# Kernel optimization log

Measured on AMD Instinct MI355X. Metric: run time of the kernel, lower is better.

## Reference

```python
import jax, jax.numpy as jnp
import numpy as np

BLOCK_SIZE = 32
BITS = 4
Q_MAX = 2 ** (BITS - 1) - 1  # 7


def setup_inputs() -> dict:
    key = jax.random.key(0)
    k1, k2, k3, k4 = jax.random.split(key, 4)
    B, S, D_in, D_out = 4, 2048, 4096, 4096
    x = jax.random.normal(k1, (B, S, D_in), dtype=jnp.float32)
    # 4-bit symmetric quantized values in [-8, 7], stored as int32
    weight_q = jax.random.randint(k2, (D_out, D_in), -(2 ** (BITS - 1)), 2 ** (BITS - 1), dtype=jnp.int32)
    # per-block positive scales (abs-max of each block in the original)
    block_scales = jax.random.uniform(k3, (D_out, D_in // BLOCK_SIZE), dtype=jnp.float32, minval=0.01, maxval=1.0)
    bias = jax.random.normal(k4, (D_out,), dtype=jnp.float32) * 0.01
    return {"x": x, "weight_q": weight_q, "block_scales": block_scales, "bias": bias}


def _dequantize(weight_q, block_scales):
    out_f, in_f = weight_q.shape
    n_blocks = in_f // BLOCK_SIZE
    q = weight_q.reshape(out_f, n_blocks, BLOCK_SIZE).astype(jnp.float32)
    w = q / Q_MAX * block_scales[:, :, None]
    return w.reshape(out_f, in_f)


def reference(x, weight_q, block_scales, bias):
    # block dequantize: w = q / q_max * scale, then y = x @ w.T + b
    w = _dequantize(weight_q, block_scales)  # [out, in] fp32
    return jnp.einsum('bsi,oi->bso', x, w) + bias
```

## Files before the change

kernel.cpp:

```cpp
#include <hip/hip_runtime.h>
#include <stdint.h>

#define M_DIM 8192
#define N_DIM 4096
#define K_DIM 4096
#define NBLK  (K_DIM / 32)

typedef __attribute__((ext_vector_type(4)))  float          f32x4;
typedef __attribute__((ext_vector_type(16))) float          f32x16;
typedef __attribute__((ext_vector_type(8)))  short          bf16x8;
typedef __attribute__((ext_vector_type(4)))  int            i32x4;
typedef __attribute__((ext_vector_type(8)))  unsigned short u16x8;
typedef __attribute__((address_space(3)))    unsigned short lds_us;

__device__ __forceinline__ unsigned short f2bf(float f) {
  unsigned u = __builtin_bit_cast(unsigned, f);
  u += 0x7fffu + ((u >> 16) & 1u);
  return (unsigned short)(u >> 16);
}

__device__ __forceinline__ void stage16(const unsigned short* g, lds_us* l) {
  __builtin_amdgcn_global_load_lds(
      (const __attribute__((address_space(1))) void*)g,
      (__attribute__((address_space(3))) void*)l, 16, 0, 0);
}

template <int OFF>
__device__ __forceinline__ bf16x8 dsr(lds_us* addr) {
  bf16x8 d;
  asm volatile("ds_read_b128 %0, %1 offset:%2" : "=v"(d) : "v"(addr), "n"(OFF));
  return d;
}


__global__ void MXFP4_dequant_kernel(const int* __restrict__ wq,
                                     const float* __restrict__ scales,
                                     unsigned short* __restrict__ wb) {
  size_t t = (size_t)blockIdx.x * 256 + threadIdx.x;
  int l  = (int)(t & 63);
  int r  = l & 31, cq = l >> 5;
  int sub = (int)(t >> 6) & 15;
  int mb = sub >> 2, ks = sub & 3;
  int H = (int)(t >> 10) & 31;
  int g = (int)(t >> 15);
  size_t row = (size_t)H * 128 + mb * 32 + r;
  size_t k   = (size_t)g * 64 + ks * 16 + cq * 8;
  float s = scales[row * NBLK + (k >> 5)] * (1.0f / 7.0f);
  const int* src = wq + row * K_DIM + k;
  i32x4 q0 = *(const i32x4*)src;
  i32x4 q1 = *(const i32x4*)(src + 4);
  u16x8 out;
#pragma unroll
  for (int j = 0; j < 4; ++j) out[j]     = f2bf((float)q0[j] * s);
#pragma unroll
  for (int j = 0; j < 4; ++j) out[4 + j] = f2bf((float)q1[j] * s);
  *(u16x8*)(wb + t * 8) = out;
}

__global__ void MXFP4_cvt_kernel(const float* __restrict__ x,
                                 unsigned short* __restrict__ xb) {
  size_t t = (size_t)blockIdx.x * 256 + threadIdx.x;
  int l  = (int)(t & 63);
  int r  = l & 31, cq = l >> 5;
  int sub = (int)(t >> 6) & 15;
  int mb = sub >> 2, ks = sub & 3;
  int H = (int)(t >> 10) & 63;
  int g = (int)(t >> 16);
  size_t row = (size_t)H * 128 + mb * 32 + r;
  size_t k   = (size_t)g * 64 + ks * 16 + cq * 8;
  const float* src = x + row * K_DIM + k;
  f32x4 v0 = *(const f32x4*)src;
  f32x4 v1 = *(const f32x4*)(src + 4);
  u16x8 out;
#pragma unroll
  for (int j = 0; j < 4; ++j) out[j]     = f2bf(v0[j]);
#pragma unroll
  for (int j = 0; j < 4; ++j) out[4 + j] = f2bf(v1[j]);
  *(u16x8*)(xb + t * 8) = out;
}


#define BAR() __builtin_amdgcn_s_barrier()
#define WAIT_LGKM(N_) do { asm volatile("s_waitcnt lgkmcnt(%0)" :: "n"(N_) : "memory"); \
                           __builtin_amdgcn_sched_barrier(0); } while (0)

#define ST_A(t_, h_, BUFA_, valid_) do { \
  if (valid_) { \
    const unsigned short* s_ = Abase + ((size_t)(t_) * 64 + (h_)) * 8192 + tid8; \
    lds_us* d_ = lp + (BUFA_) * 16384 + (h_) * 8192 + tid8; \
    stage16(s_, d_); stage16(s_ + 4096, d_ + 4096); \
  } else { stage16(Abase + tid8, lp + 65536); \
           stage16(Abase + tid8 + 4096, lp + 65536 + 512); } \
} while (0)

#define ST_B(t_, h_, BUFB_, valid_) do { \
  if (valid_) { \
    const unsigned short* s_ = Bbase + ((size_t)(t_) * 32 + (h_)) * 8192 + tid8; \
    lds_us* d_ = lp + 32768 + (BUFB_) * 16384 + (h_) * 8192 + tid8; \
    stage16(s_, d_); stage16(s_ + 4096, d_ + 4096); \
  } else { stage16(Bbase + tid8, lp + 65536); \
           stage16(Bbase + tid8 + 4096, lp + 65536 + 512); } \
} while (0)

#define MF(MB_, NB_, AF_, BF_) do { \
  _Pragma("unroll") \
  for (int ks_ = 0; ks_ < 4; ++ks_) \
    _Pragma("unroll") \
    for (int mm_ = 0; mm_ < 2; ++mm_) \
      acc[(MB_) + mm_][NB_] = __builtin_amdgcn_mfma_f32_32x32x16_bf16( \
          AF_[mm_][ks_], BF_[ks_], acc[(MB_) + mm_][NB_], 0, 0, 0); \
} while (0)

#define RD_ALO_BLO(dsA_, dsB_) do { \
  aLo[0][0] = dsr<0>(dsA_);      aLo[0][1] = dsr<1024>(dsA_); \
  aLo[0][2] = dsr<2048>(dsA_);   aLo[0][3] = dsr<3072>(dsA_); \
  aLo[1][0] = dsr<4096>(dsA_);   aLo[1][1] = dsr<5120>(dsA_); \
  aLo[1][2] = dsr<6144>(dsA_);   aLo[1][3] = dsr<7168>(dsA_); \
  bLo[0] = dsr<0>(dsB_);         bLo[1] = dsr<1024>(dsB_); \
  bLo[2] = dsr<2048>(dsB_);      bLo[3] = dsr<3072>(dsB_); \
} while (0)

#define GROUP(BUF_, tB_, tA_, vB_, vA_, RDN_) do { \
  lds_us* dsA_ = lp + (BUF_) * 16384 + wm * 8192 + lane * 8; \
  lds_us* dsB_ = lp + 32768 + (BUF_) * 16384 + wn * 4096 + lane * 8; \
  lds_us* dsA2_ = lp + ((BUF_) ^ 1) * 16384 + wm * 8192 + lane * 8; \
  lds_us* dsB2_ = lp + 32768 + ((BUF_) ^ 1) * 16384 + wn * 4096 + lane * 8; \
   \
  aHi[0][0] = dsr<8192>(dsA_);   aHi[0][1] = dsr<9216>(dsA_); \
  aHi[0][2] = dsr<10240>(dsA_);  aHi[0][3] = dsr<11264>(dsA_); \
  aHi[1][0] = dsr<12288>(dsA_);  aHi[1][1] = dsr<13312>(dsA_); \
  aHi[1][2] = dsr<14336>(dsA_);  aHi[1][3] = dsr<15360>(dsA_); \
  ST_B(tB_, 0, (BUF_) ^ 1, vB_); \
  BAR(); WAIT_LGKM(8);  \
  __builtin_amdgcn_s_setprio(1); \
  MF(0, 0, aLo, bLo); \
  __builtin_amdgcn_s_setprio(0); \
  BAR(); \
   \
  bHi[0] = dsr<4096>(dsB_);      bHi[1] = dsr<5120>(dsB_); \
  bHi[2] = dsr<6144>(dsB_);      bHi[3] = dsr<7168>(dsB_); \
  ST_B(tB_, 1, (BUF_) ^ 1, vB_); \
  BAR(); WAIT_LGKM(4);  \
  __builtin_amdgcn_s_setprio(1); \
  MF(2, 0, aHi, bLo); \
  __builtin_amdgcn_s_setprio(0); \
  BAR(); \
   \
  ST_A(tA_, 0, (BUF_), vA_); \
  BAR(); WAIT_LGKM(0);  \
  __builtin_amdgcn_s_setprio(1); \
  MF(0, 1, aLo, bHi); \
  __builtin_amdgcn_s_setprio(0); \
  BAR(); \
   \
  ST_A(tA_, 1, (BUF_), vA_); \
  asm volatile("s_waitcnt vmcnt(4)" ::: "memory"); \
  BAR(); \
  if (RDN_) { RD_ALO_BLO(dsA2_, dsB2_); } \
  __builtin_amdgcn_s_setprio(1); \
  MF(2, 1, aHi, bHi); \
  __builtin_amdgcn_s_setprio(0); \
  BAR(); \
} while (0)

__global__ __launch_bounds__(512, 2) void MXFP4_gemm_kernel(
    const unsigned short* __restrict__ A,
    const unsigned short* __restrict__ B,
    const float* __restrict__ bias,
    float* __restrict__ C) {
  __shared__ unsigned short LDS[66560];
  lds_us* lp = (lds_us*)LDS;

  const int tid  = threadIdx.x;
  const int lane = tid & 63;
  const int wv   = tid >> 6;
  const int wm   = wv >> 2;
  const int wn   = wv & 3;
  const int tid8 = tid * 8;

  const int bid = blockIdx.x;
  const int xcd = bid & 7;
  const int idx = bid >> 3;
  const int tm  = (xcd & 3) * 8 + (idx & 7);
  const int tn  = (xcd >> 2) * 8 + (idx >> 3);
  const int brow = tm * 256;
  const int bcol = tn * 256;

  const unsigned short* Abase = A + (size_t)(tm * 2) * 8192;
  const unsigned short* Bbase = B + (size_t)(tn * 2) * 8192;

  f32x16 acc[4][2] = {};
  bf16x8 aLo[2][4], aHi[2][4], bLo[4], bHi[4];

  ST_A(0, 0, 0, true); ST_A(0, 1, 0, true);
  ST_B(0, 0, 0, true); ST_B(0, 1, 0, true);
  ST_A(1, 0, 1, true); ST_A(1, 1, 1, true);
  asm volatile("s_waitcnt vmcnt(4)" ::: "memory");
  BAR();
  {
    lds_us* dsA0 = lp + wm * 8192 + lane * 8;
    lds_us* dsB0 = lp + 32768 + wn * 4096 + lane * 8;
    RD_ALO_BLO(dsA0, dsB0);
  }

  for (int it = 0; it < 31; ++it) {
    const int g0 = 2 * it;
    GROUP(0, g0 + 1, g0 + 2, true, true, true);
    GROUP(1, g0 + 2, g0 + 3, true, true, true);
  }
  GROUP(0, 63, 64, true, false, true);
  GROUP(1, 64, 65, false, false, false);

  const int rb = brow + wm * 128 + 4 * (lane >> 5);
  const int cb = bcol + wn * 64 + (lane & 31);
#pragma unroll
  for (int nb = 0; nb < 2; ++nb) {
    const int col = cb + nb * 32;
    const float bv = bias[col];
#pragma unroll
    for (int mb = 0; mb < 4; ++mb) {
      const int rowb = rb + mb * 32;
#pragma unroll
      for (int rg = 0; rg < 16; ++rg) {
        const int row = rowb + (rg & 3) + 8 * (rg >> 2);
        C[(size_t)row * N_DIM + col] = acc[mb][nb][rg] + bv;
      }
    }
  }
}

extern "C" void kernel_launch(void* const* d_in, const int* in_sizes, int n_in,
                              void* d_out, int out_size, void* d_ws, size_t ws_size,
                              hipStream_t stream) {
  const float* x      = (const float*)d_in[0];
  const int*   wq     = (const int*)d_in[1];
  const float* scales = (const float*)d_in[2];
  const float* bias   = (const float*)d_in[3];
  float*       out    = (float*)d_out;

  unsigned short* wb = (unsigned short*)d_ws;
  unsigned short* xb = wb + (size_t)N_DIM * K_DIM;

  MXFP4_dequant_kernel<<<(N_DIM * (long)K_DIM / 8) / 256, 256, 0, stream>>>(wq, scales, wb);
  MXFP4_cvt_kernel<<<(M_DIM * (long)K_DIM / 8) / 256, 256, 0, stream>>>(x, xb);

  MXFP4_gemm_kernel<<<512, 512, 0, stream>>>(xb, wb, bias, out);
}
```

Measured before the change: 312.5 us.

## Load B fragments directly from global into registers, stage only A through LDS

The GEMM main loop stops staging the weight (B) tiles through LDS. Each wave now reads its B fragments straight from global memory into double-buffered registers, while A is still staged in LDS and the MFMA phases are regrouped into two per stage. The aim is to halve LDS footprint and LDS read traffic and to cut barriers per K step. In exchange it raises VGPR pressure, and B loads are no longer shared across the waves in a workgroup, which duplicates global and L2 traffic and risks exposed global latency.

```diff
diff --git a/kernel.cpp b/kernel.cpp
--- a/kernel.cpp
+++ b/kernel.cpp
@@ -29,6 +29,14 @@
 __device__ __forceinline__ bf16x8 dsr(lds_us* addr) {
   bf16x8 d;
   asm volatile("ds_read_b128 %0, %1 offset:%2" : "=v"(d) : "v"(addr), "n"(OFF));
+  return d;
+}
+
+template <int OFF>
+__device__ __forceinline__ bf16x8 gld(const unsigned short* addr) {
+  bf16x8 d;
+  asm volatile("global_load_dwordx4 %0, %1, off offset:%2"
+               : "=v"(d) : "v"(addr), "n"(OFF));
   return d;
 }
 
@@ -81,86 +89,71 @@
 
 
 #define BAR() __builtin_amdgcn_s_barrier()
-#define WAIT_LGKM(N_) do { asm volatile("s_waitcnt lgkmcnt(%0)" :: "n"(N_) : "memory"); \
-                           __builtin_amdgcn_sched_barrier(0); } while (0)
-
-#define ST_A(t_, h_, BUFA_, valid_) do { \
+#define WAIT_LGKM0() do { asm volatile("s_waitcnt lgkmcnt(0)" ::: "memory"); \
+                          __builtin_amdgcn_sched_barrier(0); } while (0)
+
+#define ST_A_LO(t_, BUFA_, valid_) do { \
   if (valid_) { \
-    const unsigned short* s_ = Abase + ((size_t)(t_) * 64 + (h_)) * 8192 + tid8; \
-    lds_us* d_ = lp + (BUFA_) * 16384 + (h_) * 8192 + tid8; \
-    stage16(s_, d_); stage16(s_ + 4096, d_ + 4096); \
-  } else { stage16(Abase + tid8, lp + 65536); \
-           stage16(Abase + tid8 + 4096, lp + 65536 + 512); } \
-} while (0)
-
-#define ST_B(t_, h_, BUFB_, valid_) do { \
+    stage16(Abase + (size_t)(t_) * 524288 + tid8,        lp + (BUFA_) * 16384 + tid8); \
+    stage16(Abase + (size_t)(t_) * 524288 + 8192 + tid8, lp + (BUFA_) * 16384 + 8192 + tid8); \
+  } else { stage16(Abase + tid8, lp + 32768); \
+           stage16(Abase + tid8, lp + 32768 + 512); } \
+} while (0)
+
+#define ST_A_HI(t_, BUFA_, valid_) do { \
   if (valid_) { \
-    const unsigned short* s_ = Bbase + ((size_t)(t_) * 32 + (h_)) * 8192 + tid8; \
-    lds_us* d_ = lp + 32768 + (BUFB_) * 16384 + (h_) * 8192 + tid8; \
-    stage16(s_, d_); stage16(s_ + 4096, d_ + 4096); \
-  } else { stage16(Bbase + tid8, lp + 65536); \
-           stage16(Bbase + tid8 + 4096, lp + 65536 + 512); } \
-} while (0)
-
-#define MF(MB_, NB_, AF_, BF_) do { \
+    stage16(Abase + (size_t)(t_) * 524288 + 4096 + tid8,  lp + (BUFA_) * 16384 + 4096 + tid8); \
+    stage16(Abase + (size_t)(t_) * 524288 + 12288 + tid8, lp + (BUFA_) * 16384 + 12288 + tid8); \
+  } else { stage16(Abase + tid8, lp + 32768); \
+           stage16(Abase + tid8, lp + 32768 + 512); } \
+} while (0)
+
+#define MF(MB_, NB_, AF_, BFP_) do { \
   _Pragma("unroll") \
   for (int ks_ = 0; ks_ < 4; ++ks_) \
     _Pragma("unroll") \
     for (int mm_ = 0; mm_ < 2; ++mm_) \
       acc[(MB_) + mm_][NB_] = __builtin_amdgcn_mfma_f32_32x32x16_bf16( \
-          AF_[mm_][ks_], BF_[ks_], acc[(MB_) + mm_][NB_], 0, 0, 0); \
-} while (0)
-
-#define RD_ALO_BLO(dsA_, dsB_) do { \
-  aLo[0][0] = dsr<0>(dsA_);      aLo[0][1] = dsr<1024>(dsA_); \
-  aLo[0][2] = dsr<2048>(dsA_);   aLo[0][3] = dsr<3072>(dsA_); \
-  aLo[1][0] = dsr<4096>(dsA_);   aLo[1][1] = dsr<5120>(dsA_); \
-  aLo[1][2] = dsr<6144>(dsA_);   aLo[1][3] = dsr<7168>(dsA_); \
-  bLo[0] = dsr<0>(dsB_);         bLo[1] = dsr<1024>(dsB_); \
-  bLo[2] = dsr<2048>(dsB_);      bLo[3] = dsr<3072>(dsB_); \
-} while (0)
-
-#define GROUP(BUF_, tB_, tA_, vB_, vA_, RDN_) do { \
-  lds_us* dsA_ = lp + (BUF_) * 16384 + wm * 8192 + lane * 8; \
-  lds_us* dsB_ = lp + 32768 + (BUF_) * 16384 + wn * 4096 + lane * 8; \
+          AF_[mm_][ks_], (BFP_)[ks_], acc[(MB_) + mm_][NB_], 0, 0, 0); \
+} while (0)
+
+#define RD_A(dsb_, HO_) do { \
+  aF[0][0] = dsr<(HO_) + 0>(dsb_);    aF[0][1] = dsr<(HO_) + 1024>(dsb_); \
+  aF[0][2] = dsr<(HO_) + 2048>(dsb_); aF[0][3] = dsr<(HO_) + 3072>(dsb_); \
+  aF[1][0] = dsr<(HO_) + 4096>(dsb_); aF[1][1] = dsr<(HO_) + 5120>(dsb_); \
+  aF[1][2] = dsr<(HO_) + 6144>(dsb_); aF[1][3] = dsr<(HO_) + 7168>(dsb_); \
+} while (0)
+
+#define GLD_B(R_, t_, valid_) do { \
+  const unsigned short* pb_ = (valid_) ? (Bw + (size_t)(t_) * 262144) : Bw; \
+  R_[0] = gld<0>(pb_);    R_[1] = gld<1024>(pb_); \
+  R_[2] = gld<2048>(pb_); R_[3] = gld<3072>(pb_); \
+  const unsigned short* pb2_ = pb_ + 2048; \
+  R_[4] = gld<0>(pb2_);    R_[5] = gld<1024>(pb2_); \
+  R_[6] = gld<2048>(pb2_); R_[7] = gld<3072>(pb2_); \
+} while (0)
+
+#define GROUP(BUF_, BC_, BN_, tN_, vN_, tL_, vL_, RDN_) do { \
+  lds_us* dsA_  = lp + (BUF_) * 16384 + wm * 8192 + lane * 8; \
   lds_us* dsA2_ = lp + ((BUF_) ^ 1) * 16384 + wm * 8192 + lane * 8; \
-  lds_us* dsB2_ = lp + 32768 + ((BUF_) ^ 1) * 16384 + wn * 4096 + lane * 8; \
    \
-  aHi[0][0] = dsr<8192>(dsA_);   aHi[0][1] = dsr<9216>(dsA_); \
-  aHi[0][2] = dsr<10240>(dsA_);  aHi[0][3] = dsr<11264>(dsA_); \
-  aHi[1][0] = dsr<12288>(dsA_);  aHi[1][1] = dsr<13312>(dsA_); \
-  aHi[1][2] = dsr<14336>(dsA_);  aHi[1][3] = dsr<15360>(dsA_); \
-  ST_B(tB_, 0, (BUF_) ^ 1, vB_); \
-  BAR(); WAIT_LGKM(8);  \
+  GLD_B(BN_, tN_, vN_); \
+  ST_A_HI(tN_, (BUF_) ^ 1, vN_); \
+  WAIT_LGKM0();  \
   __builtin_amdgcn_s_setprio(1); \
-  MF(0, 0, aLo, bLo); \
+  MF(0, 0, aF, BC_); MF(0, 1, aF, (BC_) + 4); \
   __builtin_amdgcn_s_setprio(0); \
+  RD_A(dsA_, 8192);   \
   BAR(); \
    \
-  bHi[0] = dsr<4096>(dsB_);      bHi[1] = dsr<5120>(dsB_); \
-  bHi[2] = dsr<6144>(dsB_);      bHi[3] = dsr<7168>(dsB_); \
-  ST_B(tB_, 1, (BUF_) ^ 1, vB_); \
-  BAR(); WAIT_LGKM(4);  \
+  ST_A_LO(tL_, (BUF_), vL_); \
+  WAIT_LGKM0();  \
   __builtin_amdgcn_s_setprio(1); \
-  MF(2, 0, aHi, bLo); \
+  MF(2, 0, aF, BC_); MF(2, 1, aF, (BC_) + 4); \
   __builtin_amdgcn_s_setprio(0); \
+  asm volatile("s_waitcnt vmcnt(2)" ::: "memory");  \
   BAR(); \
-   \
-  ST_A(tA_, 0, (BUF_), vA_); \
-  BAR(); WAIT_LGKM(0);  \
-  __builtin_amdgcn_s_setprio(1); \
-  MF(0, 1, aLo, bHi); \
-  __builtin_amdgcn_s_setprio(0); \
-  BAR(); \
-   \
-  ST_A(tA_, 1, (BUF_), vA_); \
-  asm volatile("s_waitcnt vmcnt(4)" ::: "memory"); \
-  BAR(); \
-  if (RDN_) { RD_ALO_BLO(dsA2_, dsB2_); } \
-  __builtin_amdgcn_s_setprio(1); \
-  MF(2, 1, aHi, bHi); \
-  __builtin_amdgcn_s_setprio(0); \
-  BAR(); \
+  if (RDN_) { RD_A(dsA2_, 0); }  \
 } while (0)
 
 __global__ __launch_bounds__(512, 2) void MXFP4_gemm_kernel(
@@ -168,7 +161,7 @@
     const unsigned short* __restrict__ B,
     const float* __restrict__ bias,
     float* __restrict__ C) {
-  __shared__ unsigned short LDS[66560];
+  __shared__ unsigned short LDS[33792];
   lds_us* lp = (lds_us*)LDS;
 
   const int tid  = threadIdx.x;
@@ -187,29 +180,28 @@
   const int bcol = tn * 256;
 
   const unsigned short* Abase = A + (size_t)(tm * 2) * 8192;
-  const unsigned short* Bbase = B + (size_t)(tn * 2) * 8192;
+  const unsigned short* Bw =
+      B + (size_t)(tn * 2 + (wn >> 1)) * 8192 + (wn & 1) * 4096 + lane * 8;
 
   f32x16 acc[4][2] = {};
-  bf16x8 aLo[2][4], aHi[2][4], bLo[4], bHi[4];
-
-  ST_A(0, 0, 0, true); ST_A(0, 1, 0, true);
-  ST_B(0, 0, 0, true); ST_B(0, 1, 0, true);
-  ST_A(1, 0, 1, true); ST_A(1, 1, 1, true);
-  asm volatile("s_waitcnt vmcnt(4)" ::: "memory");
+  bf16x8 aF[2][4];
+  bf16x8 b0[8], b1[8];
+
+  ST_A_LO(0, 0, true); ST_A_HI(0, 0, true);
+  GLD_B(b0, 0, true);
+  ST_A_LO(1, 1, true);
+  asm volatile("s_waitcnt vmcnt(2)" ::: "memory");
   BAR();
-  {
-    lds_us* dsA0 = lp + wm * 8192 + lane * 8;
-    lds_us* dsB0 = lp + 32768 + wn * 4096 + lane * 8;
-    RD_ALO_BLO(dsA0, dsB0);
-  }
+  { lds_us* dsA0 = lp + wm * 8192 + lane * 8;
+    RD_A(dsA0, 0); }
 
   for (int it = 0; it < 31; ++it) {
     const int g0 = 2 * it;
-    GROUP(0, g0 + 1, g0 + 2, true, true, true);
-    GROUP(1, g0 + 2, g0 + 3, true, true, true);
+    GROUP(0, b0, b1, g0 + 1, true, g0 + 2, true, true);
+    GROUP(1, b1, b0, g0 + 2, true, g0 + 3, true, true);
   }
-  GROUP(0, 63, 64, true, false, true);
-  GROUP(1, 64, 65, false, false, false);
+  GROUP(0, b0, b1, 63, true, 64, false, true);
+  GROUP(1, b1, b0, 64, false, 65, false, false);
 
   const int rb = brow + wm * 128 + 4 * (lane >> 5);
   const int cb = bcol + wn * 64 + (lane & 31);
```

Result: slower. 323.0 us (+3.3%).
